# Kernel tuning notes

Measured on AMD Instinct MI355X. Metric: run time of the kernel, lower is better.

Reference implementation:

```python
import jax, jax.numpy as jnp
import numpy as np

H = 16  # number of heads

def setup_inputs() -> dict:
    key = jax.random.key(0)
    ks = jax.random.split(key, 9)
    B, N, D = 2, 2048, 1024
    s = 0.02
    q = jax.random.normal(ks[0], (B, N, D), jnp.float32)
    k = jax.random.normal(ks[1], (B, N, D), jnp.float32)
    v = jax.random.normal(ks[2], (B, N, D), jnp.float32)
    mask = jax.random.randint(ks[3], (B, 1, N, N), 0, 2).astype(bool)
    Wq = jax.random.normal(ks[4], (D, D), jnp.float32) * s
    Wk = jax.random.normal(ks[5], (D, D), jnp.float32) * s
    Wv = jax.random.normal(ks[6], (D, D), jnp.float32) * s
    Wo = jax.random.normal(ks[7], (D, D), jnp.float32) * s
    bq = jnp.zeros((D,), jnp.float32)
    bk = jnp.zeros((D,), jnp.float32)
    bv = jnp.zeros((D,), jnp.float32)
    bo = jnp.zeros((D,), jnp.float32)
    return {"q": q, "k": k, "v": v, "mask": mask,
            "Wq": Wq, "bq": bq, "Wk": Wk, "bk": bk,
            "Wv": Wv, "bv": bv, "Wo": Wo, "bo": bo}


def reference(q, k, v, mask, Wq, bq, Wk, bk, Wv, bv, Wo, bo):
    B, N, D = q.shape
    dk = D // H
    # nn.Linear: x @ W.T + b, then split heads: b n (h d) -> b h n d
    def proj(x, W, b):
        return (x @ W.T + b).reshape(B, N, H, dk).transpose(0, 2, 1, 3)
    qh = proj(q, Wq, bq)  # [B,H,N,dk]
    kh = proj(k, Wk, bk)
    vh = proj(v, Wv, bv)
    # NOTE: original has NO 1/sqrt(dk) scaling
    score = jnp.einsum('bhnd,bhmd->bhnm', qh, kh)
    score = jnp.where(mask, jnp.float32(-1e9), score)
    attn = jax.nn.softmax(score, axis=-1)
    x = jnp.einsum('bhnm,bhmd->bhnd', attn, vh)
    x = x.transpose(0, 2, 1, 3).reshape(B, N, D)  # b h n d -> b n (h d)
    return x @ Wo.T + bo
```

## Files before the change

### kernel.cpp

```cpp
#include <hip/hip_runtime.h>
#include <math.h>

#define BB 2
#define NN 2048
#define DD 1024
#define HH 16
#define DK 64
#define LOG2E 1.4426950408889634f

typedef __attribute__((ext_vector_type(8))) short short8;
typedef __attribute__((ext_vector_type(4))) float f32x4;
typedef __attribute__((ext_vector_type(16))) float f32x16;
typedef __attribute__((ext_vector_type(4))) float f32x4v;
typedef __attribute__((ext_vector_type(8))) unsigned short ushort8;
typedef unsigned long long u64;

__device__ __forceinline__ unsigned short f2bf(float f) {
  unsigned u = __float_as_uint(f);
  unsigned r = (u + 0x7FFFu + ((u >> 16) & 1u)) >> 16;
  return (unsigned short)r;
}

__device__ __forceinline__ void gload_lds16(const void* g, void* l) {
  auto gp = (const __attribute__((address_space(1))) unsigned int*)(unsigned long long)g;
  auto lp = (__attribute__((address_space(3))) unsigned int*)(unsigned int)(unsigned long long)l;
  __builtin_amdgcn_global_load_lds(gp, lp, 16, 0, 0);
}

__global__ __launch_bounds__(256) void cvt_all(
    const float* __restrict__ q, const float* __restrict__ k, const float* __restrict__ v,
    const float* __restrict__ wq, const float* __restrict__ wk, const float* __restrict__ wv,
    const float* __restrict__ wo, unsigned short* __restrict__ ws)
{
  const long NW = (long)DD * DD;
  const long NX = (long)BB * NN * DD;
  long i = ((long)blockIdx.x * blockDim.x + threadIdx.x) * 8;
  if (i >= 4 * NW + 3 * NX) return;
  const float* src; unsigned short* dst; long off;
  if (i < 4 * NW) {
    int s = (int)(i / NW);
    src = (s == 0) ? wq : (s == 1) ? wk : (s == 2) ? wv : wo;
    off = i - (long)s * NW;
    dst = ws + (long)s * NW + off;
  } else {
    long j = i - 4 * NW;
    int s = (int)(j / NX);
    src = (s == 0) ? q : (s == 1) ? k : v;
    off = j - (long)s * NX;
    dst = ws + 4 * NW + (long)s * NX + off;
  }
  f32x4v a = *(const f32x4v*)(src + off);
  f32x4v b = *(const f32x4v*)(src + off + 4);
  ushort8 o;
  o[0] = f2bf(a[0]); o[1] = f2bf(a[1]); o[2] = f2bf(a[2]); o[3] = f2bf(a[3]);
  o[4] = f2bf(b[0]); o[5] = f2bf(b[1]); o[6] = f2bf(b[2]); o[7] = f2bf(b[3]);
  *(ushort8*)dst = o;
}

__global__ __launch_bounds__(256) void cvt_mask_bits(const void* __restrict__ mask,
                                                     u64* __restrict__ mb, long total64)
{
  const unsigned char* m8 = (const unsigned char*)mask;
  const int l = threadIdx.x & 63;
  unsigned probe = m8[l * 4 + 1] | m8[l * 4 + 2] | m8[l * 4 + 3];
  const bool isBool = (__any(probe != 0) != 0);

  long t = (long)blockIdx.x * blockDim.x + threadIdx.x;
  if (t >= total64) return;
  u64 bits = 0;
  if (isBool) {
    const uint4* p = (const uint4*)(m8 + t * 64);
#pragma unroll
    for (int i = 0; i < 4; ++i) {
      uint4 q4 = p[i];
      unsigned vv[4] = {q4.x, q4.y, q4.z, q4.w};
#pragma unroll
      for (int j = 0; j < 4; ++j)
#pragma unroll
        for (int bb = 0; bb < 4; ++bb)
          bits |= (u64)((vv[j] >> (8 * bb)) & 1u) << (i * 16 + j * 4 + bb);
    }
  } else {
    const int4* p = (const int4*)((const int*)mask + t * 64);
#pragma unroll
    for (int i = 0; i < 16; ++i) {
      int4 q4 = p[i];
      bits |= (u64)(q4.x & 1) << (i * 4);
      bits |= (u64)(q4.y & 1) << (i * 4 + 1);
      bits |= (u64)(q4.z & 1) << (i * 4 + 2);
      bits |= (u64)(q4.w & 1) << (i * 4 + 3);
    }
  }
  const long bb2 = t >> 16;
  const long qq = (t >> 5) & 2047;
  const long tcol = t & 31;
  mb[(bb2 * 32 + tcol) * 2048 + qq] = bits;
}

struct GemmArgs {
  const unsigned short* A;
  const unsigned short* Bw;
  const float* bias;
  void* C;
  int mode;
  float oscale;
};

template<int TM>
__global__ __launch_bounds__(256) void gemm_bt(GemmArgs ga0, GemmArgs ga1, GemmArgs ga2)
{
  constexpr int K = DD;
  constexpr int Nn = DD;
  constexpr int PERZ_LOG = (TM == 128) ? 8 : 9;
  constexpr int NF = (TM == 128) ? 4 : 2;
  __shared__ __align__(16) unsigned short As[TM * 32];
  __shared__ __align__(16) unsigned short Bs[128 * 32];

  const int gy = (TM == 128) ? 32 : 64;
  int wgid = blockIdx.x + ((blockIdx.y + blockIdx.z * gy) << 3);
  const int nwg = (int)gridDim.z << PERZ_LOG;
  const int chunk = nwg >> 3;
  wgid = (wgid & 7) * chunk + (wgid >> 3);
  const int zi = wgid >> PERZ_LOG;
  const int rem = wgid & ((1 << PERZ_LOG) - 1);
  const int m0 = (rem >> 3) * TM;
  const int n0 = (rem & 7) * 128;
  GemmArgs ga = (zi == 0) ? ga0 : ((zi == 1) ? ga1 : ga2);

  const int tid = threadIdx.x;
  const int lane = tid & 63;
  const int w = tid >> 6;
  const int m_woff = (TM == 128) ? (w >> 1) * 64 : 0;
  const int n_woff = (TM == 128) ? (w & 1) * 64 : w * 32;
  const int c = lane & 15, g = lane >> 4;

  f32x4 acc[4][NF];
  const f32x4 z4 = {0.f, 0.f, 0.f, 0.f};
#pragma unroll
  for (int m = 0; m < 4; ++m)
#pragma unroll
    for (int n = 0; n < NF; ++n) acc[m][n] = z4;

  const unsigned short* Ab = ga.A + (long)m0 * K;
  const unsigned short* Bb = ga.Bw + (long)n0 * K;
  const int ar = tid >> 2;
  const int ac = (tid & 3) * 8;

  for (int kk = 0; kk < K; kk += 32) {
#pragma unroll
    for (int i = 0; i < TM / 64; ++i)
      gload_lds16(Ab + (long)(i * 64 + ar) * K + kk + ac, &As[i * 2048 + tid * 8]);
#pragma unroll
    for (int i = 0; i < 2; ++i)
      gload_lds16(Bb + (long)(i * 64 + ar) * K + kk + ac, &Bs[i * 2048 + tid * 8]);
    __syncthreads();

    short8 a[4], b[NF];
#pragma unroll
    for (int m = 0; m < 4; ++m)
      a[m] = *(const short8*)&As[(m_woff + 16 * m + c) * 32 + g * 8];
#pragma unroll
    for (int n = 0; n < NF; ++n)
      b[n] = *(const short8*)&Bs[(n_woff + 16 * n + c) * 32 + g * 8];
#pragma unroll
    for (int m = 0; m < 4; ++m)
#pragma unroll
      for (int n = 0; n < NF; ++n)
        acc[m][n] = __builtin_amdgcn_mfma_f32_16x16x32_bf16(a[m], b[n], acc[m][n], 0, 0, 0);
    __syncthreads();
  }

#pragma unroll
  for (int n = 0; n < NF; ++n) {
    const int col = n0 + n_woff + 16 * n + c;
    const float bv = ga.bias[col];
#pragma unroll
    for (int m = 0; m < 4; ++m) {
      const int row0 = m0 + m_woff + 16 * m + 4 * g;
#pragma unroll
      for (int r = 0; r < 4; ++r) {
        const int row = row0 + r;
        const float val = (acc[m][n][r] + bv) * ga.oscale;
        if (ga.mode == 1)
          ((float*)ga.C)[(long)row * Nn + col] = val;
        else if (ga.mode == 0)
          ((unsigned short*)ga.C)[(long)row * Nn + col] = f2bf(val);
        else
          ((unsigned short*)ga.C)[((long)(row >> 11) * DD + col) * NN + (row & (NN - 1))] = f2bf(val);
      }
    }
  }
}

__global__ __launch_bounds__(256, 2) void attn_kernel(
    const unsigned short* __restrict__ Q,
    const unsigned short* __restrict__ K,
    const unsigned short* __restrict__ Vt,
    const u64* __restrict__ mb64,
    unsigned short* __restrict__ ctx)
{
  __shared__ __align__(16) unsigned short Ks[2][64 * 64];
  __shared__ __align__(16) unsigned short Vs[2][64 * 64];

  const int tid = threadIdx.x;
  const int lane = tid & 63;
  const int w = tid >> 6;
  const int bid = blockIdx.x;
  const int b = (bid >> 4) & 1, h = bid & 15;
  const int q0 = (bid >> 5) * 128;
  const int l31 = lane & 31;
  const int hi = lane >> 5;
  const int qrow = q0 + 32 * w + l31;

  short8 aq[4];
  {
    const unsigned short* qp = Q + ((long)(b * NN + qrow)) * DD + h * DK + 8 * hi;
    aq[0] = *(const short8*)(qp);
    aq[1] = *(const short8*)(qp + 16);
    aq[2] = *(const short8*)(qp + 32);
    aq[3] = *(const short8*)(qp + 48);
  }

  f32x16 o0, o1, cinit;
#pragma unroll
  for (int r = 0; r < 16; ++r) { o0[r] = 0.f; o1[r] = 0.f; cinit[r] = -28.853901f; }
  float lsum = 0.f;

  const unsigned short* Kbase = K + (long)(b * NN) * DD + h * DK;
  const unsigned short* Vbase = Vt + ((long)(b * DD + h * DK)) * NN;
  const u64* mbase = mb64 + (long)(b * 32) * 2048 + qrow;

  const int srow = tid >> 3;
  const int scol = tid & 7;
  const int swcol = scol ^ (srow & 7);

  auto STAGE = [&](int buf, int t) {
#pragma unroll
    for (int hf = 0; hf < 2; ++hf) {
      const int row = srow + 32 * hf;
      gload_lds16(Kbase + (long)(t * 64 + row) * DD + swcol * 8, &Ks[buf][hf * 2048 + tid * 8]);
      gload_lds16(Vbase + (long)row * NN + t * 64 + swcol * 8, &Vs[buf][hf * 2048 + tid * 8]);
    }
  };

  STAGE(0, 0);
  __syncthreads();
  int cur = 0;
  const int sh4 = 4 * hi;
  u64 mword = mbase[0];

  for (int t = 0; t < 32; ++t) {
    const u64 mnext = (t < 31) ? mbase[(long)(t + 1) * 2048] : 0;
    if (t < 31) STAGE(cur ^ 1, t + 1);
    const unsigned msk0 = ((unsigned)mword) >> sh4;
    const unsigned msk1 = ((unsigned)(mword >> 32)) >> sh4;

#pragma unroll
    for (int sub = 0; sub < 2; ++sub) {
      const unsigned m = sub ? msk1 : msk0;
      const int krow = l31 + 32 * sub;
      const int kswz = (krow & 7) << 3;

      f32x16 ss = cinit;
      __builtin_amdgcn_s_setprio(1);
#pragma unroll
      for (int i = 0; i < 4; ++i) {
        const short8 kf = *(const short8*)&Ks[cur][krow * 64 + ((16 * i + 8 * hi) ^ kswz)];
        ss = __builtin_amdgcn_mfma_f32_32x32x16_bf16(kf, aq[i], ss, 0, 0, 0);
      }
      __builtin_amdgcn_s_setprio(0);

      float p[16];
#pragma unroll
      for (int r = 0; r < 16; ++r) {
        const int cr = (r & 3) + 8 * (r >> 2);
        const float e = ((m >> cr) & 1u) ? -1e9f : ss[r];
        p[r] = __builtin_amdgcn_exp2f(e);
        lsum += p[r];
      }

      unsigned wv[8];
#pragma unroll
      for (int i = 0; i < 8; ++i) {
        unsigned rr;
        asm("v_cvt_pk_bf16_f32 %0, %1, %2" : "=v"(rr) : "v"(p[2 * i]), "v"(p[2 * i + 1]));
        wv[i] = rr;
      }
      asm("v_permlane32_swap_b32 %0, %1" : "+v"(wv[0]), "+v"(wv[2]));
      asm("v_permlane32_swap_b32 %0, %1" : "+v"(wv[1]), "+v"(wv[3]));
      asm("v_permlane32_swap_b32 %0, %1" : "+v"(wv[4]), "+v"(wv[6]));
      asm("v_permlane32_swap_b32 %0, %1" : "+v"(wv[5]), "+v"(wv[7]));
      union { short8 s; unsigned u[4]; } pa0, pa1;
      pa0.u[0] = wv[0]; pa0.u[1] = wv[1]; pa0.u[2] = wv[2]; pa0.u[3] = wv[3];
      pa1.u[0] = wv[4]; pa1.u[1] = wv[5]; pa1.u[2] = wv[6]; pa1.u[3] = wv[7];

      __builtin_amdgcn_s_setprio(1);
#pragma unroll
      for (int dblk = 0; dblk < 2; ++dblk) {
        const int vrow = l31 + 32 * dblk;
        const int vswz = (vrow & 7) << 3;
        const short8 vb0 = *(const short8*)&Vs[cur][vrow * 64 + ((32 * sub + 8 * hi) ^ vswz)];
        const short8 vb1 = *(const short8*)&Vs[cur][vrow * 64 + ((32 * sub + 16 + 8 * hi) ^ vswz)];
        if (dblk == 0) {
          o0 = __builtin_amdgcn_mfma_f32_32x32x16_bf16(pa0.s, vb0, o0, 0, 0, 0);
          o0 = __builtin_amdgcn_mfma_f32_32x32x16_bf16(pa1.s, vb1, o0, 0, 0, 0);
        } else {
          o1 = __builtin_amdgcn_mfma_f32_32x32x16_bf16(pa0.s, vb0, o1, 0, 0, 0);
          o1 = __builtin_amdgcn_mfma_f32_32x32x16_bf16(pa1.s, vb1, o1, 0, 0, 0);
        }
      }
      __builtin_amdgcn_s_setprio(0);
    }
    __syncthreads();
    cur ^= 1;
    mword = mnext;
  }

  lsum += __shfl_xor(lsum, 32);
  const float inv = 1.0f / lsum;

#pragma unroll
  for (int r = 0; r < 16; ++r) {
    const int qr = (r & 3) + 8 * (r >> 2) + 4 * hi;
    const float linv = __shfl(inv, qr);
    const long row = (long)(b * NN + q0 + 32 * w + qr);
    ctx[row * DD + h * DK + l31] = f2bf(o0[r] * linv);
    ctx[row * DD + h * DK + 32 + l31] = f2bf(o1[r] * linv);
  }
}

extern "C" void kernel_launch(void* const* d_in, const int* in_sizes, int n_in,
                              void* d_out, int out_size, void* d_ws, size_t ws_size,
                              hipStream_t stream) {
  const float* q  = (const float*)d_in[0];
  const float* k  = (const float*)d_in[1];
  const float* v  = (const float*)d_in[2];
  const void*  mask = d_in[3];
  const float* Wq = (const float*)d_in[4];
  const float* bq = (const float*)d_in[5];
  const float* Wk = (const float*)d_in[6];
  const float* bk = (const float*)d_in[7];
  const float* Wv = (const float*)d_in[8];
  const float* bv = (const float*)d_in[9];
  const float* Wo = (const float*)d_in[10];
  const float* bo = (const float*)d_in[11];

  unsigned short* ws = (unsigned short*)d_ws;
  const long NW = (long)DD * DD;
  const long NX = (long)BB * NN * DD;
  unsigned short* Wqb = ws;
  unsigned short* Wkb = ws + NW;
  unsigned short* Wvb = ws + 2 * NW;
  unsigned short* Wob = ws + 3 * NW;
  unsigned short* Xq  = ws + 4 * NW;
  unsigned short* Xk  = Xq + NX;
  unsigned short* Xv  = Xk + NX;
  unsigned short* Qh  = Xv + NX;
  unsigned short* Kh  = Qh + NX;
  unsigned short* Vtr = Kh + NX;
  unsigned short* Ctx = Vtr + NX;
  u64* Mbits = (u64*)(Ctx + NX);
  const long NM64 = (long)BB * NN * NN / 64;

  cvt_all<<<8192, 256, 0, stream>>>(q, k, v, Wq, Wk, Wv, Wo, ws);
  cvt_mask_bits<<<(int)(NM64 / 256), 256, 0, stream>>>(mask, Mbits, NM64);

  GemmArgs gq = {Xq, Wqb, bq, (void*)Qh, 0, LOG2E};
  GemmArgs gk = {Xk, Wkb, bk, (void*)Kh, 0, 1.0f};
  GemmArgs gv = {Xv, Wvb, bv, (void*)Vtr, 2, 1.0f};
  dim3 gproj(DD / 128, (BB * NN) / 128, 3);
  gemm_bt<128><<<gproj, 256, 0, stream>>>(gq, gk, gv);

  attn_kernel<<<512, 256, 0, stream>>>(Qh, Kh, Vtr, Mbits, Ctx);

  GemmArgs go = {Ctx, Wob, bo, d_out, 1, 1.0f};
  dim3 gout(DD / 128, (BB * NN) / 64, 1);
  gemm_bt<64><<<gout, 256, 0, stream>>>(go, go, go);
}
```

Baseline: 146.6 us.

## Double-buffer GEMM LDS tiles with XOR swizzle and MFMA priority boost

The projection GEMM now uses two LDS buffers, so the global-to-LDS load of the next K tile is issued before the MFMAs on the current tile run. That overlaps memory latency with compute and cuts one barrier per iteration. It also XOR-swizzles the LDS column layout to reduce bank conflicts on the short8 reads, and raises wave priority around the MFMA block. In exchange, LDS use doubles, which may lower occupancy, and correctness now depends on the hand-placed waitcnt and barrier ordering.

```diff
diff --git a/kernel.cpp b/kernel.cpp
--- a/kernel.cpp
+++ b/kernel.cpp
@@ -113,8 +113,9 @@
   constexpr int Nn = DD;
   constexpr int PERZ_LOG = (TM == 128) ? 8 : 9;
   constexpr int NF = (TM == 128) ? 4 : 2;
-  __shared__ __align__(16) unsigned short As[TM * 32];
-  __shared__ __align__(16) unsigned short Bs[128 * 32];
+  constexpr int NT = K / 32;
+  __shared__ __align__(16) unsigned short As[2][TM * 32];
+  __shared__ __align__(16) unsigned short Bs[2][128 * 32];
 
   const int gy = (TM == 128) ? 32 : 64;
   int wgid = blockIdx.x + ((blockIdx.y + blockIdx.z * gy) << 3);
@@ -144,30 +145,49 @@
   const unsigned short* Ab = ga.A + (long)m0 * K;
   const unsigned short* Bb = ga.Bw + (long)n0 * K;
   const int ar = tid >> 2;
-  const int ac = (tid & 3) * 8;
-
-  for (int kk = 0; kk < K; kk += 32) {
+  const int ac = ((tid & 3) ^ (ar & 3)) * 8;
+
+  auto STAGE = [&](int buf, int kk) {
 #pragma unroll
     for (int i = 0; i < TM / 64; ++i)
-      gload_lds16(Ab + (long)(i * 64 + ar) * K + kk + ac, &As[i * 2048 + tid * 8]);
+      gload_lds16(Ab + (long)(i * 64 + ar) * K + kk + ac, &As[buf][i * 2048 + tid * 8]);
 #pragma unroll
     for (int i = 0; i < 2; ++i)
-      gload_lds16(Bb + (long)(i * 64 + ar) * K + kk + ac, &Bs[i * 2048 + tid * 8]);
-    __syncthreads();
+      gload_lds16(Bb + (long)(i * 64 + ar) * K + kk + ac, &Bs[buf][i * 2048 + tid * 8]);
+  };
+
+  STAGE(0, 0);
+  asm volatile("s_waitcnt vmcnt(0)" ::: "memory");
+  __builtin_amdgcn_s_barrier();
+  __builtin_amdgcn_sched_barrier(0);
+  int cur = 0;
+
+  const int rswz = (g ^ (c & 3)) * 8;
+
+  for (int t = 0; t < NT; ++t) {
+    if (t + 1 < NT) STAGE(cur ^ 1, (t + 1) * 32);
 
     short8 a[4], b[NF];
 #pragma unroll
     for (int m = 0; m < 4; ++m)
-      a[m] = *(const short8*)&As[(m_woff + 16 * m + c) * 32 + g * 8];
+      a[m] = *(const short8*)&As[cur][(m_woff + 16 * m + c) * 32 + rswz];
 #pragma unroll
     for (int n = 0; n < NF; ++n)
-      b[n] = *(const short8*)&Bs[(n_woff + 16 * n + c) * 32 + g * 8];
+      b[n] = *(const short8*)&Bs[cur][(n_woff + 16 * n + c) * 32 + rswz];
+    __builtin_amdgcn_s_setprio(1);
 #pragma unroll
     for (int m = 0; m < 4; ++m)
 #pragma unroll
       for (int n = 0; n < NF; ++n)
         acc[m][n] = __builtin_amdgcn_mfma_f32_16x16x32_bf16(a[m], b[n], acc[m][n], 0, 0, 0);
-    __syncthreads();
+    __builtin_amdgcn_s_setprio(0);
+
+    if (t + 1 < NT) {
+      asm volatile("s_waitcnt vmcnt(0)" ::: "memory");
+      __builtin_amdgcn_s_barrier();
+      __builtin_amdgcn_sched_barrier(0);
+      cur ^= 1;
+    }
   }
 
 #pragma unroll
```

Result: slower. 149.6 us (+2.1%).
